# Kernel optimization log

Hardware: AMD Instinct MI355X
Metric: run time of the kernel (lower is better)

The kernel has to match this reference:

```python
import jax, jax.numpy as jnp
import numpy as np

H = 512   # lstm_hidden_size
B = 64    # batch
S = 256   # seqlen


def setup_inputs() -> dict:
    key = jax.random.key(0)
    ks = jax.random.split(key, 6)
    scale = 1.0 / np.sqrt(H)  # PyTorch LSTM default init range
    return {
        "x": jax.random.normal(ks[0], (B, S, 2 * H), dtype=jnp.float32),
        "hi": jax.random.normal(ks[1], (B, S, 2 * H), dtype=jnp.float32),
        "W_ih": jax.random.uniform(ks[2], (4 * H, 5 * H), minval=-scale, maxval=scale, dtype=jnp.float32),
        "W_hh": jax.random.uniform(ks[3], (4 * H, H), minval=-scale, maxval=scale, dtype=jnp.float32),
        "b_ih": jax.random.uniform(ks[4], (4 * H,), minval=-scale, maxval=scale, dtype=jnp.float32),
        "b_hh": jax.random.uniform(ks[5], (4 * H,), minval=-scale, maxval=scale, dtype=jnp.float32),
    }


def _forward(x, hi, W_ih, W_hh, b_ih, b_hh):
    h_dim = W_hh.shape[1]
    bias = b_ih + b_hh
    xc = jnp.concatenate([x, hi], axis=-1)          # [B, S, 4H]
    xc = jnp.transpose(xc, (1, 0, 2))               # [S, B, 4H]
    batch = xc.shape[1]

    def cell(hc, inp_b):
        # inp_b: [5H]; PyTorch LSTM treats the batch dim as seq (batch_first=False quirk)
        h, c = hc
        gates = inp_b @ W_ih.T + h @ W_hh.T + bias  # [4H]
        i_g, f_g, g_g, o_g = jnp.split(gates, 4)
        i_g = jax.nn.sigmoid(i_g)
        f_g = jax.nn.sigmoid(f_g)
        g_g = jnp.tanh(g_g)
        o_g = jax.nn.sigmoid(o_g)
        c = f_g * c + i_g * g_g
        h = o_g * jnp.tanh(c)
        return (h, c), h

    def step(carry, x_i):
        out_prev, h, c = carry                      # out_prev: [B, H]
        inp = jnp.concatenate([x_i, out_prev], axis=-1)  # [B, 5H]
        (h, c), outs = jax.lax.scan(cell, (h, c), inp)    # scan over batch dim
        return (outs, h, c), outs

    init = (jnp.zeros((batch, h_dim), x.dtype),
            jnp.zeros((h_dim,), x.dtype),
            jnp.zeros((h_dim,), x.dtype))
    _, all_out = jax.lax.scan(step, init, xc)       # [S, B, H]
    return jnp.transpose(all_out, (1, 0, 2))        # [B, S, H]


def reference(x, hi, W_ih, W_hh, b_ih, b_hh):
    # Dropout layers are identity in eval mode.
    return _forward(x, hi, W_ih, W_hh, b_ih, b_hh)
```

## Files before the change

### kernel.cpp

```cpp
#include <hip/hip_runtime.h>

typedef _Float16 f16;
typedef _Float16 f16x2 __attribute__((ext_vector_type(2)));
typedef _Float16 f16x4 __attribute__((ext_vector_type(4)));
typedef _Float16 f16x8 __attribute__((ext_vector_type(8)));
typedef float f32x4 __attribute__((ext_vector_type(4)));
typedef unsigned int u32;
typedef unsigned int u32x4 __attribute__((ext_vector_type(4)));
typedef unsigned long long ull;

#define HD 512
#define T_TOT 16384
#define RING 128
#define NWG 32
#define NTH 576

static const size_t O_XC    = 0;
static const size_t O_W1    = 67108864;
static const size_t O_WHH   = 75497472;
static const size_t O_W2    = 77594624;
static const size_t O_G     = 79691776;
static const size_t O_PRING = 213909504;

__device__ __forceinline__ float dot2f(f16x2 a, f16x2 b, float c) {
#if __has_builtin(__builtin_amdgcn_fdot2)
    return __builtin_amdgcn_fdot2(a, b, c, false);
#else
    return fmaf((float)a[0], (float)b[0], fmaf((float)a[1], (float)b[1], c));
#endif
}
__device__ __forceinline__ f16x2 bcf(u32 u) { return __builtin_bit_cast(f16x2, u); }

__device__ __forceinline__ float sigf(float x) {
    return __frcp_rn(1.0f + __expf(-x));
}
__device__ __forceinline__ float tanhfast(float x) {
    return 1.0f - 2.0f * __frcp_rn(__expf(2.0f * x) + 1.0f);
}

__device__ __forceinline__ ull ld_a64(const ull* p) {
    return __hip_atomic_load(p, __ATOMIC_RELAXED, __HIP_MEMORY_SCOPE_AGENT);
}
__device__ __forceinline__ void st_a64(ull* p, ull v) {
    __hip_atomic_store(p, v, __ATOMIC_RELAXED, __HIP_MEMORY_SCOPE_AGENT);
}

__global__ __launch_bounds__(256) void conv_xc(const float* __restrict__ x,
                                               const float* __restrict__ hi,
                                               f16* __restrict__ xc) {
    int gid = blockIdx.x * 256 + threadIdx.x;
    int t = gid >> 9;
    int k = (gid & 511) << 2;
    int b = t & 63, s = t >> 6;
    const float* src = (k < 1024) ? (x  + ((size_t)((b << 8) + s) << 10) + k)
                                  : (hi + ((size_t)((b << 8) + s) << 10) + (k - 1024));
    float4 v = *reinterpret_cast<const float4*>(src);
    f16x4 o = { (_Float16)v.x, (_Float16)v.y, (_Float16)v.z, (_Float16)v.w };
    *reinterpret_cast<f16x4*>(xc + ((size_t)t << 11) + k) = o;
}

__global__ __launch_bounds__(256) void conv_w1(const float* __restrict__ wih,
                                               f16* __restrict__ w1) {
    int gid = blockIdx.x * 256 + threadIdx.x;
    int j = gid >> 9;
    int k = (gid & 511) << 2;
    float4 v = *reinterpret_cast<const float4*>(wih + (size_t)j * 2560 + k);
    f16x4 o = { (_Float16)v.x, (_Float16)v.y, (_Float16)v.z, (_Float16)v.w };
    *reinterpret_cast<f16x4*>(w1 + ((size_t)j << 11) + k) = o;
}

__global__ __launch_bounds__(256) void conv_wc(const float* __restrict__ whh,
                                               const float* __restrict__ wih,
                                               f16* __restrict__ whhf,
                                               f16* __restrict__ w2f) {
    int gid = blockIdx.x * 256 + threadIdx.x;
    int j = gid >> 7;
    int k = (gid & 127) << 2;
    float4 a = *reinterpret_cast<const float4*>(whh + (size_t)j * 512 + k);
    f16x4 oa = { (_Float16)a.x, (_Float16)a.y, (_Float16)a.z, (_Float16)a.w };
    *reinterpret_cast<f16x4*>(whhf + ((size_t)j << 9) + k) = oa;
    float4 bv = *reinterpret_cast<const float4*>(wih + (size_t)j * 2560 + 2048 + k);
    f16x4 ob = { (_Float16)bv.x, (_Float16)bv.y, (_Float16)bv.z, (_Float16)bv.w };
    *reinterpret_cast<f16x4*>(w2f + ((size_t)j << 9) + k) = ob;
}

__global__ __launch_bounds__(256) void gemm_pre(const f16* __restrict__ XC,
                                                const f16* __restrict__ W1,
                                                const float* __restrict__ b_ih,
                                                const float* __restrict__ b_hh,
                                                float* __restrict__ G) {
    int w = threadIdx.x >> 6, l = threadIdx.x & 63;
    int R0 = blockIdx.y * 128 + (w >> 1) * 64;
    int C0 = blockIdx.x * 128 + (w & 1) * 64;
    int lr = l & 15, kb = l >> 4;
    f32x4 acc[4][4] = {};
    const f16* Abase = XC + (size_t)(R0 + lr) * 2048 + kb * 8;
    const f16* Bbase = W1 + (size_t)(C0 + lr) * 2048 + kb * 8;
    for (int kk = 0; kk < 2048; kk += 32) {
        f16x8 av[4], bv[4];
#pragma unroll
        for (int i = 0; i < 4; i++)
            av[i] = *reinterpret_cast<const f16x8*>(Abase + (size_t)(i * 16) * 2048 + kk);
#pragma unroll
        for (int i = 0; i < 4; i++)
            bv[i] = *reinterpret_cast<const f16x8*>(Bbase + (size_t)(i * 16) * 2048 + kk);
#pragma unroll
        for (int fr = 0; fr < 4; fr++)
#pragma unroll
            for (int fc = 0; fc < 4; fc++)
                acc[fr][fc] = __builtin_amdgcn_mfma_f32_16x16x32_f16(av[fr], bv[fc], acc[fr][fc], 0, 0, 0);
    }
#pragma unroll
    for (int fc = 0; fc < 4; fc++) {
        int col = C0 + fc * 16 + lr;
        float bias = b_ih[col] + b_hh[col];
#pragma unroll
        for (int fr = 0; fr < 4; fr++) {
#pragma unroll
            for (int r = 0; r < 4; r++) {
                int row = R0 + fr * 16 + kb * 4 + r;
                G[(size_t)row * 2048 + col] = acc[fr][fc][r] + bias;
            }
        }
    }
}

__global__ __launch_bounds__(NTH, 1) void lstm_chain(const float* __restrict__ G,
                                                     const f16* __restrict__ Whhf,
                                                     const f16* __restrict__ W2f,
                                                     ull* __restrict__ ring,
                                                     float* __restrict__ out) {
    const int wg = blockIdx.x;
    const int tid = threadIdx.x;
    const int wv = tid >> 6, l = tid & 63;

    __shared__ u32x4 hist[RING][64];
    __shared__ float part[2][4][16];

    for (int i = tid; i < 64 * 64; i += NTH)
        hist[64 + (i >> 6)][i & 63] = (u32x4){0u, 0u, 0u, 0u};

    u32 wu1[32], wu2[32];
    if (wv < 8) {
        const int g = wv & 3, uh = wv >> 2;
        const int row0 = g * 512 + wg * 16 + uh * 8;
#pragma unroll
        for (int r = 0; r < 8; r++) {
            f16x8 v1 = *reinterpret_cast<const f16x8*>(Whhf + (size_t)(row0 + r) * 512 + 8 * l);
            f16x8 v2 = *reinterpret_cast<const f16x8*>(W2f  + (size_t)(row0 + r) * 512 + 8 * l);
            u32x4 a = __builtin_bit_cast(u32x4, v1);
            u32x4 b = __builtin_bit_cast(u32x4, v2);
            wu1[r * 4 + 0] = a.x; wu1[r * 4 + 1] = a.y; wu1[r * 4 + 2] = a.z; wu1[r * 4 + 3] = a.w;
            wu2[r * 4 + 0] = b.x; wu2[r * 4 + 1] = b.y; wu2[r * 4 + 2] = b.z; wu2[r * 4 + 3] = b.w;
        }
#pragma unroll
        for (int i = 0; i < 32; i++) {
            asm volatile("" : "+v"(wu1[i]));
            asm volatile("" : "+v"(wu2[i]));
        }
    }

    const int g = wv & 3, uh = wv >> 2;
    const int grow = (l >> 4) * 512 + wg * 16 + (l & 15);
    float gval = 0.0f, cst = 0.0f;
    if (wv == 8) gval = G[grow];
    __syncthreads();

    for (int t = 0; t < T_TOT; t++) {
        const int buf = t & 1;
        const int sA = (t + 64) & (RING - 1);
        const int sB = (t - 1) & (RING - 1);
        const int sW = t & (RING - 1);

        float a[8] = {0.f, 0.f, 0.f, 0.f, 0.f, 0.f, 0.f, 0.f};
        float gn = gval;

        if (wv < 8) {
            u32x4 ch = hist[sA][l];
            f16x2 h0 = bcf(ch.x), h1 = bcf(ch.y), h2 = bcf(ch.z), h3 = bcf(ch.w);
#pragma unroll
            for (int r = 0; r < 8; r++) {
                a[r] = dot2f(bcf(wu2[r * 4 + 0]), h0, a[r]);
                a[r] = dot2f(bcf(wu2[r * 4 + 1]), h1, a[r]);
                a[r] = dot2f(bcf(wu2[r * 4 + 2]), h2, a[r]);
                a[r] = dot2f(bcf(wu2[r * 4 + 3]), h3, a[r]);
            }
        } else {
            int tn = (t + 1 < T_TOT) ? t + 1 : t;
            gn = G[(size_t)tn * 2048 + grow];
            const ull* base = ring + (size_t)sB * 256 + 4 * l;
            const u32 want = (u32)t;
            ull v0, v1, v2, v3;
            while (true) {
                v0 = ld_a64(base + 0);
                v1 = ld_a64(base + 1);
                v2 = ld_a64(base + 2);
                v3 = ld_a64(base + 3);
                u32 x = ((u32)(v0 >> 32) ^ want) | ((u32)(v1 >> 32) ^ want) |
                        ((u32)(v2 >> 32) ^ want) | ((u32)(v3 >> 32) ^ want);
                if (__all(x == 0)) break;
            }
            hist[sB][l] = (u32x4){(u32)v0, (u32)v1, (u32)v2, (u32)v3};
        }
        __syncthreads();

        if (wv < 8) {
            u32x4 ch = hist[sB][l];
            f16x2 h0 = bcf(ch.x), h1 = bcf(ch.y), h2 = bcf(ch.z), h3 = bcf(ch.w);
#pragma unroll
            for (int r = 0; r < 8; r++) {
                a[r] = dot2f(bcf(wu1[r * 4 + 0]), h0, a[r]);
                a[r] = dot2f(bcf(wu1[r * 4 + 1]), h1, a[r]);
                a[r] = dot2f(bcf(wu1[r * 4 + 2]), h2, a[r]);
                a[r] = dot2f(bcf(wu1[r * 4 + 3]), h3, a[r]);
            }
            const bool s0 = l & 1, s1 = l & 2, s2 = l & 4;
            float b4_0 = (s0 ? a[4] : a[0]) + __shfl_xor((s0 ? a[0] : a[4]), 1);
            float b4_1 = (s0 ? a[5] : a[1]) + __shfl_xor((s0 ? a[1] : a[5]), 1);
            float b4_2 = (s0 ? a[6] : a[2]) + __shfl_xor((s0 ? a[2] : a[6]), 1);
            float b4_3 = (s0 ? a[7] : a[3]) + __shfl_xor((s0 ? a[3] : a[7]), 1);
            float c2_0 = (s1 ? b4_2 : b4_0) + __shfl_xor((s1 ? b4_0 : b4_2), 2);
            float c2_1 = (s1 ? b4_3 : b4_1) + __shfl_xor((s1 ? b4_1 : b4_3), 2);
            float d    = (s2 ? c2_1 : c2_0) + __shfl_xor((s2 ? c2_0 : c2_1), 4);
            d += __shfl_xor(d, 8);
            d += __shfl_xor(d, 16);
            d += __shfl_xor(d, 32);
            if (l < 8) {
                int rr = ((l & 1) << 2) | (l & 2) | ((l >> 2) & 1);
                part[buf][g][uh * 8 + rr] = d;
            }
        }
        __syncthreads();

        if (wv == 8) {
            int gg = l >> 4, uu = l & 15;
            float val = part[buf][gg][uu] + gval;
            float act = (gg == 2) ? tanhfast(val) : sigf(val);
            float fi = __shfl(act, uu);
            float ff = __shfl(act, uu + 16);
            float fg = __shfl(act, uu + 32);
            float fo = __shfl(act, uu + 48);
            cst = ff * cst + fi * fg;
            float h = fo * tanhfast(cst);
            u32 hb = (u32)__builtin_bit_cast(unsigned short, (f16)h);
            u32 plo = (u32)__shfl((int)hb, 2 * (l & 7));
            u32 phi = (u32)__shfl((int)hb, 2 * (l & 7) + 1);
            ull pv = (ull)(plo & 0xffffu) | ((ull)(phi & 0xffffu) << 16) |
                     ((ull)(u32)(t + 1) << 32);
            if (l < 8)
                st_a64(ring + (size_t)sW * 256 + wg * 8 + l, pv);
            if (l < 16) {
                int b = t & 63, s = t >> 6;
                out[((size_t)((b << 8) + s)) * 512 + wg * 16 + l] = h;
            }
        }
        gval = gn;
    }
}

extern "C" void kernel_launch(void* const* d_in, const int* in_sizes, int n_in,
                              void* d_out, int out_size, void* d_ws, size_t ws_size,
                              hipStream_t stream) {
    const float* x    = (const float*)d_in[0];
    const float* hi   = (const float*)d_in[1];
    const float* W_ih = (const float*)d_in[2];
    const float* W_hh = (const float*)d_in[3];
    const float* b_ih = (const float*)d_in[4];
    const float* b_hh = (const float*)d_in[5];

    char* ws = (char*)d_ws;
    f16*   XCf   = (f16*)(ws + O_XC);
    f16*   W1f   = (f16*)(ws + O_W1);
    f16*   Whhf  = (f16*)(ws + O_WHH);
    f16*   W2f   = (f16*)(ws + O_W2);
    float* G     = (float*)(ws + O_G);
    ull*   ring  = (ull*)(ws + O_PRING);

    hipMemsetAsync(ring, 0, (size_t)RING * 256 * sizeof(ull), stream);

    conv_xc<<<32768, 256, 0, stream>>>(x, hi, XCf);
    conv_w1<<<4096, 256, 0, stream>>>(W_ih, W1f);
    conv_wc<<<1024, 256, 0, stream>>>(W_hh, W_ih, Whhf, W2f);
    gemm_pre<<<dim3(16, 128), 256, 0, stream>>>(XCf, W1f, b_ih, b_hh, G);
    lstm_chain<<<NWG, NTH, 0, stream>>>(G, Whhf, W2f, ring, (float*)d_out);
}
```

Baseline: 29.49 ms.

## Poll ring directly in compute waves, dropping one barrier per step

Each of the 8 compute waves now spins on the global ring itself and uses the loaded hidden state straight from registers. Previously a dedicated wave polled the ring, staged the data in LDS, and then a block barrier released the compute waves. This removes one __syncthreads per timestep from the serial critical path. The gate preactivation prefetch moves into an LDS double buffer that the idle wave fills two steps ahead, and the history layout and gate activations are restructured so each of 16 lanes handles one unit. The trade is eight waves hammering the same global ring lines while they poll, which adds memory traffic and contention.

```diff
diff --git a/kernel.cpp b/kernel.cpp
--- a/kernel.cpp
+++ b/kernel.cpp
@@ -31,12 +31,8 @@
 }
 __device__ __forceinline__ f16x2 bcf(u32 u) { return __builtin_bit_cast(f16x2, u); }
 
-__device__ __forceinline__ float sigf(float x) {
-    return __frcp_rn(1.0f + __expf(-x));
-}
-__device__ __forceinline__ float tanhfast(float x) {
-    return 1.0f - 2.0f * __frcp_rn(__expf(2.0f * x) + 1.0f);
-}
+__device__ __forceinline__ float sigf(float x) { return 1.0f / (1.0f + __expf(-x)); }
+__device__ __forceinline__ float tanhfast(float x) { return 1.0f - 2.0f / (__expf(2.0f * x) + 1.0f); }
 
 __device__ __forceinline__ ull ld_a64(const ull* p) {
     return __hip_atomic_load(p, __ATOMIC_RELAXED, __HIP_MEMORY_SCOPE_AGENT);
@@ -133,128 +129,121 @@
     const int wg = blockIdx.x;
     const int tid = threadIdx.x;
     const int wv = tid >> 6, l = tid & 63;
-
-    __shared__ u32x4 hist[RING][64];
-    __shared__ float part[2][4][16];
-
-    for (int i = tid; i < 64 * 64; i += NTH)
-        hist[64 + (i >> 6)][i & 63] = (u32x4){0u, 0u, 0u, 0u};
+    const int g = wv & 3, uh = (wv >> 2) & 3;
+    const int rr = ((l & 1) << 2) | (l & 2) | ((l >> 2) & 1);
+    const int row0 = g * 512 + wg * 16 + uh * 8;
+
+    __shared__ u32 hist[64][256];
+    __shared__ float part[2][16][4];
+    __shared__ float gbuf[2][64];
+
+    for (int i = tid; i < 4096; i += NTH)
+        reinterpret_cast<u32x4*>(hist)[i] = (u32x4){0u, 0u, 0u, 0u};
 
     u32 wu1[32], wu2[32];
-    if (wv < 8) {
-        const int g = wv & 3, uh = wv >> 2;
-        const int row0 = g * 512 + wg * 16 + uh * 8;
-#pragma unroll
-        for (int r = 0; r < 8; r++) {
-            f16x8 v1 = *reinterpret_cast<const f16x8*>(Whhf + (size_t)(row0 + r) * 512 + 8 * l);
-            f16x8 v2 = *reinterpret_cast<const f16x8*>(W2f  + (size_t)(row0 + r) * 512 + 8 * l);
-            u32x4 a = __builtin_bit_cast(u32x4, v1);
-            u32x4 b = __builtin_bit_cast(u32x4, v2);
-            wu1[r * 4 + 0] = a.x; wu1[r * 4 + 1] = a.y; wu1[r * 4 + 2] = a.z; wu1[r * 4 + 3] = a.w;
-            wu2[r * 4 + 0] = b.x; wu2[r * 4 + 1] = b.y; wu2[r * 4 + 2] = b.z; wu2[r * 4 + 3] = b.w;
-        }
-#pragma unroll
-        for (int i = 0; i < 32; i++) {
-            asm volatile("" : "+v"(wu1[i]));
-            asm volatile("" : "+v"(wu2[i]));
-        }
-    }
-
-    const int g = wv & 3, uh = wv >> 2;
-    const int grow = (l >> 4) * 512 + wg * 16 + (l & 15);
-    float gval = 0.0f, cst = 0.0f;
-    if (wv == 8) gval = G[grow];
+#pragma unroll
+    for (int r = 0; r < 8; r++) {
+        u32x4 a = __builtin_bit_cast(u32x4,
+            *reinterpret_cast<const f16x8*>(Whhf + (size_t)(row0 + r) * 512 + 8 * l));
+        u32x4 b = __builtin_bit_cast(u32x4,
+            *reinterpret_cast<const f16x8*>(W2f + (size_t)(row0 + r) * 512 + 8 * l));
+        wu1[r * 4 + 0] = a.x; wu1[r * 4 + 1] = a.y; wu1[r * 4 + 2] = a.z; wu1[r * 4 + 3] = a.w;
+        wu2[r * 4 + 0] = b.x; wu2[r * 4 + 1] = b.y; wu2[r * 4 + 2] = b.z; wu2[r * 4 + 3] = b.w;
+    }
+#pragma unroll
+    for (int i = 0; i < 32; i++)
+        asm volatile("" : "+v"(wu1[i]), "+v"(wu2[i]));
+
+    const int gidx = (l >> 4) * 512 + wg * 16 + (l & 15);
+    float gv = 0.0f, cst = 0.0f;
+    if (wv == 8) {
+        gbuf[0][l] = G[gidx];
+        gv = G[(size_t)1 * 2048 + gidx];
+    }
     __syncthreads();
 
     for (int t = 0; t < T_TOT; t++) {
         const int buf = t & 1;
-        const int sA = (t + 64) & (RING - 1);
-        const int sB = (t - 1) & (RING - 1);
-        const int sW = t & (RING - 1);
-
-        float a[8] = {0.f, 0.f, 0.f, 0.f, 0.f, 0.f, 0.f, 0.f};
-        float gn = gval;
-
         if (wv < 8) {
-            u32x4 ch = hist[sA][l];
-            f16x2 h0 = bcf(ch.x), h1 = bcf(ch.y), h2 = bcf(ch.z), h3 = bcf(ch.w);
-#pragma unroll
-            for (int r = 0; r < 8; r++) {
-                a[r] = dot2f(bcf(wu2[r * 4 + 0]), h0, a[r]);
-                a[r] = dot2f(bcf(wu2[r * 4 + 1]), h1, a[r]);
-                a[r] = dot2f(bcf(wu2[r * 4 + 2]), h2, a[r]);
-                a[r] = dot2f(bcf(wu2[r * 4 + 3]), h3, a[r]);
-            }
-        } else {
-            int tn = (t + 1 < T_TOT) ? t + 1 : t;
-            gn = G[(size_t)tn * 2048 + grow];
-            const ull* base = ring + (size_t)sB * 256 + 4 * l;
+            u32x4 hv = *reinterpret_cast<const u32x4*>(&hist[t & 63][4 * l]);
+            float ac[8] = {0.f, 0.f, 0.f, 0.f, 0.f, 0.f, 0.f, 0.f};
+            {
+                f16x2 h0 = bcf(hv.x), h1 = bcf(hv.y), h2 = bcf(hv.z), h3 = bcf(hv.w);
+#pragma unroll
+                for (int r = 0; r < 8; r++) {
+                    ac[r] = dot2f(bcf(wu2[r * 4 + 0]), h0, ac[r]);
+                    ac[r] = dot2f(bcf(wu2[r * 4 + 1]), h1, ac[r]);
+                    ac[r] = dot2f(bcf(wu2[r * 4 + 2]), h2, ac[r]);
+                    ac[r] = dot2f(bcf(wu2[r * 4 + 3]), h3, ac[r]);
+                }
+            }
+            float gval = (l < 8) ? gbuf[buf][g * 16 + uh * 8 + rr] : 0.0f;
+
+            const ull* pB = ring + (size_t)((t - 1) & (RING - 1)) * 256 + 4 * l;
             const u32 want = (u32)t;
-            ull v0, v1, v2, v3;
-            while (true) {
-                v0 = ld_a64(base + 0);
-                v1 = ld_a64(base + 1);
-                v2 = ld_a64(base + 2);
-                v3 = ld_a64(base + 3);
-                u32 x = ((u32)(v0 >> 32) ^ want) | ((u32)(v1 >> 32) ^ want) |
-                        ((u32)(v2 >> 32) ^ want) | ((u32)(v3 >> 32) ^ want);
-                if (__all(x == 0)) break;
-            }
-            hist[sB][l] = (u32x4){(u32)v0, (u32)v1, (u32)v2, (u32)v3};
-        }
-        __syncthreads();
-
-        if (wv < 8) {
-            u32x4 ch = hist[sB][l];
-            f16x2 h0 = bcf(ch.x), h1 = bcf(ch.y), h2 = bcf(ch.z), h3 = bcf(ch.w);
-#pragma unroll
-            for (int r = 0; r < 8; r++) {
-                a[r] = dot2f(bcf(wu1[r * 4 + 0]), h0, a[r]);
-                a[r] = dot2f(bcf(wu1[r * 4 + 1]), h1, a[r]);
-                a[r] = dot2f(bcf(wu1[r * 4 + 2]), h2, a[r]);
-                a[r] = dot2f(bcf(wu1[r * 4 + 3]), h3, a[r]);
+            ull b0 = ld_a64(pB + 0), b1 = ld_a64(pB + 1);
+            ull b2 = ld_a64(pB + 2), b3 = ld_a64(pB + 3);
+            while ((((u32)(b0 >> 32) ^ want) | ((u32)(b1 >> 32) ^ want) |
+                    ((u32)(b2 >> 32) ^ want) | ((u32)(b3 >> 32) ^ want)) != 0u) {
+                b0 = ld_a64(pB + 0); b1 = ld_a64(pB + 1);
+                b2 = ld_a64(pB + 2); b3 = ld_a64(pB + 3);
+            }
+            if (wv == 0)
+                *reinterpret_cast<u32x4*>(&hist[(t - 1) & 63][4 * l]) =
+                    (u32x4){(u32)b0, (u32)b1, (u32)b2, (u32)b3};
+
+            {
+                f16x2 h0 = bcf((u32)b0), h1 = bcf((u32)b1), h2 = bcf((u32)b2), h3 = bcf((u32)b3);
+#pragma unroll
+                for (int r = 0; r < 8; r++) {
+                    ac[r] = dot2f(bcf(wu1[r * 4 + 0]), h0, ac[r]);
+                    ac[r] = dot2f(bcf(wu1[r * 4 + 1]), h1, ac[r]);
+                    ac[r] = dot2f(bcf(wu1[r * 4 + 2]), h2, ac[r]);
+                    ac[r] = dot2f(bcf(wu1[r * 4 + 3]), h3, ac[r]);
+                }
             }
             const bool s0 = l & 1, s1 = l & 2, s2 = l & 4;
-            float b4_0 = (s0 ? a[4] : a[0]) + __shfl_xor((s0 ? a[0] : a[4]), 1);
-            float b4_1 = (s0 ? a[5] : a[1]) + __shfl_xor((s0 ? a[1] : a[5]), 1);
-            float b4_2 = (s0 ? a[6] : a[2]) + __shfl_xor((s0 ? a[2] : a[6]), 1);
-            float b4_3 = (s0 ? a[7] : a[3]) + __shfl_xor((s0 ? a[3] : a[7]), 1);
+            float b4_0 = (s0 ? ac[4] : ac[0]) + __shfl_xor((s0 ? ac[0] : ac[4]), 1);
+            float b4_1 = (s0 ? ac[5] : ac[1]) + __shfl_xor((s0 ? ac[1] : ac[5]), 1);
+            float b4_2 = (s0 ? ac[6] : ac[2]) + __shfl_xor((s0 ? ac[2] : ac[6]), 1);
+            float b4_3 = (s0 ? ac[7] : ac[3]) + __shfl_xor((s0 ? ac[3] : ac[7]), 1);
             float c2_0 = (s1 ? b4_2 : b4_0) + __shfl_xor((s1 ? b4_0 : b4_2), 2);
             float c2_1 = (s1 ? b4_3 : b4_1) + __shfl_xor((s1 ? b4_1 : b4_3), 2);
             float d    = (s2 ? c2_1 : c2_0) + __shfl_xor((s2 ? c2_0 : c2_1), 4);
             d += __shfl_xor(d, 8);
             d += __shfl_xor(d, 16);
             d += __shfl_xor(d, 32);
-            if (l < 8) {
-                int rr = ((l & 1) << 2) | (l & 2) | ((l >> 2) & 1);
-                part[buf][g][uh * 8 + rr] = d;
-            }
+            if (l < 8)
+                part[buf][uh * 8 + rr][g] = d + gval;
+        } else {
+            gbuf[buf ^ 1][l] = gv;
+            int tf = (t + 2 < T_TOT) ? t + 2 : T_TOT - 1;
+            gv = G[(size_t)tf * 2048 + gidx];
         }
         __syncthreads();
 
         if (wv == 8) {
-            int gg = l >> 4, uu = l & 15;
-            float val = part[buf][gg][uu] + gval;
-            float act = (gg == 2) ? tanhfast(val) : sigf(val);
-            float fi = __shfl(act, uu);
-            float ff = __shfl(act, uu + 16);
-            float fg = __shfl(act, uu + 32);
-            float fo = __shfl(act, uu + 48);
-            cst = ff * cst + fi * fg;
-            float h = fo * tanhfast(cst);
+            const int u = l & 15;
+            float4 pg = *reinterpret_cast<const float4*>(part[buf][u]);
+            float h = 0.0f;
+            if (l < 16) {
+                float fi = sigf(pg.x), ff = sigf(pg.y);
+                float fg = tanhfast(pg.z), fo = sigf(pg.w);
+                cst = ff * cst + fi * fg;
+                h = fo * tanhfast(cst);
+            }
             u32 hb = (u32)__builtin_bit_cast(unsigned short, (f16)h);
             u32 plo = (u32)__shfl((int)hb, 2 * (l & 7));
             u32 phi = (u32)__shfl((int)hb, 2 * (l & 7) + 1);
             ull pv = (ull)(plo & 0xffffu) | ((ull)(phi & 0xffffu) << 16) |
                      ((ull)(u32)(t + 1) << 32);
             if (l < 8)
-                st_a64(ring + (size_t)sW * 256 + wg * 8 + l, pv);
+                st_a64(ring + (size_t)(t & (RING - 1)) * 256 + wg * 8 + l, pv);
             if (l < 16) {
                 int b = t & 63, s = t >> 6;
                 out[((size_t)((b << 8) + s)) * 512 + wg * 16 + l] = h;
             }
         }
-        gval = gn;
     }
 }
 
```

Result: slower. 42.23 ms (+43.2%).
